# Kernel tuning notes

Hardware: AMD Instinct MI355X
Metric: run time of the kernel (lower is better)

The kernel has to match this reference:

```python
import jax, jax.numpy as jnp
import numpy as np

BINS = 10  # from __init__ default


def setup_inputs() -> dict:
    key = jax.random.key(0)
    k1, k2 = jax.random.split(key)
    N, C = 65536, 512
    # binary_cross_entropy expects probabilities in (0, 1)
    pred = jax.random.uniform(k1, (N, C), dtype=jnp.float32, minval=1e-4, maxval=1.0 - 1e-4)
    # binary targets (docstring: 'Binary class target for each sample')
    target = (jax.random.uniform(k2, (N, C)) < 0.5).astype(jnp.float32)
    return {"pred": pred, "target": target, "batch_size": N}


def reference(pred, target, batch_size):
    bins = BINS
    # gradient norm g = |pred.detach() - target| (pred is detached in the original)
    g = jnp.abs(jax.lax.stop_gradient(pred) - target)
    # uniform bin edges: element falls in bin i iff i/bins <= g < (i+1)/bins,
    # last edge bumped by 1e-6 so g == 1.0 lands in the last bin -> clip.
    idx = jnp.clip(jnp.floor(g * bins).astype(jnp.int32), 0, bins - 1)  # [N, C]
    # full histogram in one pass (replaces the python loop + .item() syncs)
    counts = jax.ops.segment_sum(
        jnp.ones(g.size, dtype=jnp.float32), idx.ravel(), num_segments=bins
    )  # [bins]
    n_nonempty = jnp.sum(counts > 0).astype(pred.dtype)
    tot = jnp.asarray(batch_size, pred.dtype)
    # per-bin weight tot / num_in_bin (empty bins never indexed, clamp for safety)
    per_bin_w = tot / jnp.maximum(counts, 1.0)  # [bins]
    weights = per_bin_w[idx] / jnp.maximum(n_nonempty, 1.0)  # [N, C]
    # weighted BCE, sum reduction, divided by tot (torch clamps log at -100)
    logp = jnp.clip(jnp.log(pred), -100.0, None)
    log1mp = jnp.clip(jnp.log1p(-pred), -100.0, None)
    loss = -jnp.sum(weights * (target * logp + (1.0 - target) * log1mp)) / tot
    return loss
```

## Files before the change

kernel.cpp:

```cpp
#include <hip/hip_runtime.h>

#define NBINS 10
#define BS 256
#define TPT 16
#define TILE (BS * TPT)
#define MAXG 2048

typedef float f32x4 __attribute__((ext_vector_type(4)));

__device__ __forceinline__ void elem(float pv, float tv, float& stot,
                                     float* __restrict__ asum,
                                     unsigned long long& cnt) {
    float g = fabsf(pv - tv);
    int idx = (int)(g * 10.0f);
    float l = __log2f(1.0f - g);
    stot += l;
    cnt += 1ull << (idx * 6);
#pragma unroll
    for (int b = 0; b < NBINS - 1; ++b)
        asum[b] += (idx == b) ? l : 0.0f;
}

__device__ __forceinline__ void unpack_counts(unsigned long long cnt,
                                              float* __restrict__ fcnt) {
#pragma unroll
    for (int b = 0; b < NBINS; ++b)
        fcnt[b] += (float)((unsigned int)((cnt >> (6 * b)) & 63ull));
}

__global__ __launch_bounds__(BS, 4) void ghm_main(
        const f32x4* __restrict__ p4, const f32x4* __restrict__ t4,
        float* __restrict__ partial, int G, long long n4, long long n) {
    float asum[NBINS - 1], fcnt[NBINS];
    float stot = 0.0f;
#pragma unroll
    for (int b = 0; b < NBINS - 1; ++b) asum[b] = 0.0f;
#pragma unroll
    for (int b = 0; b < NBINS; ++b) fcnt[b] = 0.0f;

    const int tid = threadIdx.x;
    const long long span = (long long)G * TILE;

    for (long long base = (long long)blockIdx.x * TILE; base < n4; base += span) {
        unsigned long long cntA = 0ull, cntB = 0ull;
        const long long rem = n4 - base;
        if (rem >= TILE) {
            const f32x4* __restrict__ pb = p4 + base + tid;
            const f32x4* __restrict__ tb = t4 + base + tid;
#pragma unroll
            for (int j = 0; j < 4; ++j) {
                f32x4 P[4], T[4];
#pragma unroll
                for (int k = 0; k < 4; ++k) {
                    P[k] = __builtin_nontemporal_load(pb + (j * 4 + k) * BS);
                    T[k] = __builtin_nontemporal_load(tb + (j * 4 + k) * BS);
                }
                unsigned long long& c = (j & 1) ? cntB : cntA;
#pragma unroll
                for (int k = 0; k < 4; ++k) {
                    elem(P[k].x, T[k].x, stot, asum, c);
                    elem(P[k].y, T[k].y, stot, asum, c);
                    elem(P[k].z, T[k].z, stot, asum, c);
                    elem(P[k].w, T[k].w, stot, asum, c);
                }
            }
        } else {
            for (long long q = tid; q < rem; q += 2 * BS) {
                f32x4 p = __builtin_nontemporal_load(p4 + base + q);
                f32x4 t = __builtin_nontemporal_load(t4 + base + q);
                elem(p.x, t.x, stot, asum, cntA);
                elem(p.y, t.y, stot, asum, cntA);
                elem(p.z, t.z, stot, asum, cntA);
                elem(p.w, t.w, stot, asum, cntA);
            }
            for (long long q = tid + BS; q < rem; q += 2 * BS) {
                f32x4 p = __builtin_nontemporal_load(p4 + base + q);
                f32x4 t = __builtin_nontemporal_load(t4 + base + q);
                elem(p.x, t.x, stot, asum, cntB);
                elem(p.y, t.y, stot, asum, cntB);
                elem(p.z, t.z, stot, asum, cntB);
                elem(p.w, t.w, stot, asum, cntB);
            }
        }
        unpack_counts(cntA, fcnt);
        unpack_counts(cntB, fcnt);
    }

    if (blockIdx.x == 0) {
        const long long rem0 = n4 << 2;
        if (tid < (int)(n - rem0)) {
            unsigned long long ct = 0ull;
            elem(((const float*)p4)[rem0 + tid], ((const float*)t4)[rem0 + tid],
                 stot, asum, ct);
            unpack_counts(ct, fcnt);
        }
    }

    float vals[2 * NBINS];
    {
        float s9 = stot;
#pragma unroll
        for (int b = 0; b < NBINS - 1; ++b) { vals[b] = asum[b]; s9 -= asum[b]; }
        vals[NBINS - 1] = s9;
#pragma unroll
        for (int b = 0; b < NBINS; ++b) vals[NBINS + b] = fcnt[b];
    }

#pragma unroll
    for (int v = 0; v < 2 * NBINS; ++v) {
#pragma unroll
        for (int off = 32; off > 0; off >>= 1)
            vals[v] += __shfl_down(vals[v], off, 64);
    }

    __shared__ float xw[BS / 64][2 * NBINS];
    const int wid = tid >> 6, lane = tid & 63;
    if (lane == 0) {
#pragma unroll
        for (int v = 0; v < 2 * NBINS; ++v) xw[wid][v] = vals[v];
    }
    __syncthreads();
    if (tid < 2 * NBINS) {
        float s = xw[0][tid] + xw[1][tid] + xw[2][tid] + xw[3][tid];
        partial[(size_t)tid * G + blockIdx.x] = s;
    }
}

__global__ __launch_bounds__(1024) void ghm_reduce(
        const float* __restrict__ partial, int G, float* __restrict__ out) {
    __shared__ float redS[NBINS];
    __shared__ int   redC[NBINS];
    const int tid = threadIdx.x, wid = tid >> 6, lane = tid & 63;

    for (int v = wid; v < 2 * NBINS; v += 16) {
        const float* row = partial + (size_t)v * G;
        if (v < NBINS) {
            float s = 0.0f;
            for (int i = lane; i < G; i += 64) s += row[i];
#pragma unroll
            for (int off = 32; off > 0; off >>= 1) s += __shfl_down(s, off, 64);
            if (lane == 0) redS[v] = s;
        } else {
            int c = 0;
            for (int i = lane; i < G; i += 64) c += (int)(row[i] + 0.5f);
#pragma unroll
            for (int off = 32; off > 0; off >>= 1) c += __shfl_down(c, off, 64);
            if (lane == 0) redC[v - NBINS] = c;
        }
    }
    __syncthreads();
    if (tid == 0) {
        float acc = 0.0f;
        int ne = 0;
#pragma unroll
        for (int b = 0; b < NBINS; ++b) {
            int c = redC[b];
            if (c > 0) { ne += 1; acc += redS[b] / (float)c; }
        }
        const float LN2 = 0.6931471805599453f;
        out[0] = -(LN2 * acc) / (float)(ne > 0 ? ne : 1);
    }
}

extern "C" void kernel_launch(void* const* d_in, const int* in_sizes, int n_in,
                              void* d_out, int out_size, void* d_ws, size_t ws_size,
                              hipStream_t stream) {
    const float* pred   = (const float*)d_in[0];
    const float* target = (const float*)d_in[1];
    long long n = (long long)in_sizes[0];
    long long n4 = n >> 2;

    float* partial = (float*)d_ws;

    long long need = (n4 + TILE - 1) / TILE;
    long long gcap = (long long)(ws_size / (2 * NBINS * sizeof(float)));
    long long g = MAXG;
    if (g > need) g = need;
    if (g > gcap) g = gcap;
    if (g < 1) g = 1;
    int G = (int)g;

    ghm_main<<<G, BS, 0, stream>>>((const f32x4*)pred, (const f32x4*)target,
                                   partial, G, n4, n);
    ghm_reduce<<<1, 1024, 0, stream>>>(partial, G, (float*)d_out);
}
```

Measured before the change: 67.30 us.

## Software-pipeline exact-tile loads with sched barriers and simplify fallback path

When the grid covers the input exactly (one tile per block), the kernel now double-buffers two register sets, issuing the next chunk's loads before computing on the current one, with scheduling barriers to pin that order. This aims to hide global memory latency within each block's single tile. The grid-stride tile loop is replaced by a simple per-vector grid-stride fallback for sizes that don't match. The extra in-flight registers may reduce occupancy, and the fallback path unpacks counts per vector, which is slower.

```diff
diff --git a/kernel.cpp b/kernel.cpp
--- a/kernel.cpp
+++ b/kernel.cpp
@@ -2,8 +2,7 @@
 
 #define NBINS 10
 #define BS 256
-#define TPT 16
-#define TILE (BS * TPT)
+#define FPT 16
 #define MAXG 2048
 
 typedef float f32x4 __attribute__((ext_vector_type(4)));
@@ -33,57 +32,63 @@
         float* __restrict__ partial, int G, long long n4, long long n) {
     float asum[NBINS - 1], fcnt[NBINS];
     float stot = 0.0f;
+    unsigned long long cntA = 0ull, cntB = 0ull;
 #pragma unroll
     for (int b = 0; b < NBINS - 1; ++b) asum[b] = 0.0f;
 #pragma unroll
     for (int b = 0; b < NBINS; ++b) fcnt[b] = 0.0f;
 
     const int tid = threadIdx.x;
-    const long long span = (long long)G * TILE;
+    const long long gid = (long long)blockIdx.x * BS + tid;
 
-    for (long long base = (long long)blockIdx.x * TILE; base < n4; base += span) {
-        unsigned long long cntA = 0ull, cntB = 0ull;
-        const long long rem = n4 - base;
-        if (rem >= TILE) {
-            const f32x4* __restrict__ pb = p4 + base + tid;
-            const f32x4* __restrict__ tb = t4 + base + tid;
+    if (n4 == (long long)G * BS * FPT) {
+        const f32x4* __restrict__ pb = p4 + (long long)blockIdx.x * (BS * FPT) + tid;
+        const f32x4* __restrict__ tb = t4 + (long long)blockIdx.x * (BS * FPT) + tid;
+        f32x4 PA[4], TA[4], PB[4], TB[4];
+
+        auto LOAD = [&](f32x4* P, f32x4* T, int c) {
 #pragma unroll
-            for (int j = 0; j < 4; ++j) {
-                f32x4 P[4], T[4];
+            for (int k = 0; k < 4; ++k) {
+                P[k] = __builtin_nontemporal_load(pb + (c * 4 + k) * BS);
+                T[k] = __builtin_nontemporal_load(tb + (c * 4 + k) * BS);
+            }
+        };
+        auto COMP = [&](f32x4* P, f32x4* T, unsigned long long& c) {
 #pragma unroll
-                for (int k = 0; k < 4; ++k) {
-                    P[k] = __builtin_nontemporal_load(pb + (j * 4 + k) * BS);
-                    T[k] = __builtin_nontemporal_load(tb + (j * 4 + k) * BS);
-                }
-                unsigned long long& c = (j & 1) ? cntB : cntA;
-#pragma unroll
-                for (int k = 0; k < 4; ++k) {
-                    elem(P[k].x, T[k].x, stot, asum, c);
-                    elem(P[k].y, T[k].y, stot, asum, c);
-                    elem(P[k].z, T[k].z, stot, asum, c);
-                    elem(P[k].w, T[k].w, stot, asum, c);
-                }
+            for (int k = 0; k < 4; ++k) {
+                elem(P[k].x, T[k].x, stot, asum, c);
+                elem(P[k].y, T[k].y, stot, asum, c);
+                elem(P[k].z, T[k].z, stot, asum, c);
+                elem(P[k].w, T[k].w, stot, asum, c);
             }
-        } else {
-            for (long long q = tid; q < rem; q += 2 * BS) {
-                f32x4 p = __builtin_nontemporal_load(p4 + base + q);
-                f32x4 t = __builtin_nontemporal_load(t4 + base + q);
-                elem(p.x, t.x, stot, asum, cntA);
-                elem(p.y, t.y, stot, asum, cntA);
-                elem(p.z, t.z, stot, asum, cntA);
-                elem(p.w, t.w, stot, asum, cntA);
-            }
-            for (long long q = tid + BS; q < rem; q += 2 * BS) {
-                f32x4 p = __builtin_nontemporal_load(p4 + base + q);
-                f32x4 t = __builtin_nontemporal_load(t4 + base + q);
-                elem(p.x, t.x, stot, asum, cntB);
-                elem(p.y, t.y, stot, asum, cntB);
-                elem(p.z, t.z, stot, asum, cntB);
-                elem(p.w, t.w, stot, asum, cntB);
-            }
+        };
+
+        LOAD(PA, TA, 0);
+        LOAD(PB, TB, 1);
+        __builtin_amdgcn_sched_barrier(0);
+        COMP(PA, TA, cntA);
+        __builtin_amdgcn_sched_barrier(0);
+        LOAD(PA, TA, 2);
+        __builtin_amdgcn_sched_barrier(0);
+        COMP(PB, TB, cntB);
+        __builtin_amdgcn_sched_barrier(0);
+        LOAD(PB, TB, 3);
+        __builtin_amdgcn_sched_barrier(0);
+        COMP(PA, TA, cntA);
+        __builtin_amdgcn_sched_barrier(0);
+        COMP(PB, TB, cntB);
+    } else {
+        const long long nthreads = (long long)G * BS;
+        for (long long q = gid; q < n4; q += nthreads) {
+            f32x4 p = __builtin_nontemporal_load(p4 + q);
+            f32x4 t = __builtin_nontemporal_load(t4 + q);
+            unsigned long long c = 0ull;
+            elem(p.x, t.x, stot, asum, c);
+            elem(p.y, t.y, stot, asum, c);
+            elem(p.z, t.z, stot, asum, c);
+            elem(p.w, t.w, stot, asum, c);
+            unpack_counts(c, fcnt);
         }
-        unpack_counts(cntA, fcnt);
-        unpack_counts(cntB, fcnt);
     }
 
     if (blockIdx.x == 0) {
@@ -95,6 +100,9 @@
             unpack_counts(ct, fcnt);
         }
     }
+
+    unpack_counts(cntA, fcnt);
+    unpack_counts(cntB, fcnt);
 
     float vals[2 * NBINS];
     {
@@ -172,7 +180,7 @@
 
     float* partial = (float*)d_ws;
 
-    long long need = (n4 + TILE - 1) / TILE;
+    long long need = (n4 + (BS * FPT) - 1) / (BS * FPT);
     long long gcap = (long long)(ws_size / (2 * NBINS * sizeof(float)));
     long long g = MAXG;
     if (g > need) g = need;
```

Measured after the change: 66.24 us (median of 2 runs). About the same (-1.6%).
